# Optimization experiments

Measured on AMD Instinct MI355X. Metric: run time of the kernel, lower is better.

Reference implementation:

```python
import jax, jax.numpy as jnp
import numpy as np

NEG_INF = -9e15  # matches torch masked_fill value


def setup_inputs() -> dict:
    key = jax.random.key(0)
    k1, k2 = jax.random.split(key)
    N, D = 8192, 512
    cxr_feats = jax.random.normal(k1, (N, D), dtype=jnp.float32)
    ehr_feats = jax.random.normal(k2, (N, D), dtype=jnp.float32)
    temperature = jnp.float32(0.07)
    return {"cxr_feats": cxr_feats, "ehr_feats": ehr_feats, "temperature": temperature}


def reference(cxr_feats, ehr_feats, temperature):
    # Fused L2-normalize + GEMM instead of broadcast cosine_similarity.
    eps = 1e-8  # torch cosine_similarity eps default
    cxr_n = cxr_feats / jnp.maximum(jnp.linalg.norm(cxr_feats, axis=-1, keepdims=True), eps)
    ehr_n = ehr_feats / jnp.maximum(jnp.linalg.norm(ehr_feats, axis=-1, keepdims=True), eps)
    cos_sim = jnp.einsum('nd,md->nm', cxr_n, ehr_n) / temperature  # [N, N]
    N = cos_sim.shape[0]
    diag = jnp.diagonal(cos_sim)  # positives
    self_mask = jnp.eye(N, dtype=bool)
    cos_sim_neg = jnp.where(self_mask, NEG_INF, cos_sim)
    nll_1 = diag - jax.scipy.special.logsumexp(cos_sim_neg, axis=1)
    nll_2 = diag - jax.scipy.special.logsumexp(cos_sim_neg, axis=0)
    loss = -(nll_1 + nll_2).mean()
    return loss
```

## Files before the change

kernel.cpp:

```cpp
#include <hip/hip_runtime.h>
#include <hip/hip_bf16.h>

#define N_ROWS 8192
#define D_DIM  512
#define NSTEPS 8

typedef __attribute__((ext_vector_type(4))) int   i32x4;
typedef __attribute__((ext_vector_type(8))) int   i32x8;
typedef __attribute__((ext_vector_type(16))) float f32x16;

typedef const __attribute__((address_space(1))) void* gptr_t;
typedef __attribute__((address_space(3))) void* lptr_t;

static __device__ __forceinline__ void gload16(const void* g, void* l) {
    __builtin_amdgcn_global_load_lds((gptr_t)g, (lptr_t)l, 16, 0, 0);
}
#define VMCNT(n)  asm volatile("s_waitcnt vmcnt(" #n ")" ::: "memory")
#define BARRIER() __builtin_amdgcn_s_barrier()
#define SCHED0()  __builtin_amdgcn_sched_barrier(0)

__global__ void normdiag_kernel(const float* __restrict__ cxr, const float* __restrict__ ehr,
                                unsigned char* __restrict__ Ab, unsigned char* __restrict__ Bb,
                                const float* __restrict__ temp, float* __restrict__ dg) {
    const int row = blockIdx.x * 4 + (threadIdx.x >> 6);
    const int lane = threadIdx.x & 63;
    const float4* a4 = (const float4*)(cxr + (size_t)row * D_DIM + lane * 8);
    const float4* b4 = (const float4*)(ehr + (size_t)row * D_DIM + lane * 8);
    float4 a0 = a4[0], a1 = a4[1];
    float4 b0 = b4[0], b1 = b4[1];
    float sa = a0.x*a0.x + a0.y*a0.y + a0.z*a0.z + a0.w*a0.w
             + a1.x*a1.x + a1.y*a1.y + a1.z*a1.z + a1.w*a1.w;
    float sb = b0.x*b0.x + b0.y*b0.y + b0.z*b0.z + b0.w*b0.w
             + b1.x*b1.x + b1.y*b1.y + b1.z*b1.z + b1.w*b1.w;
    float dt = a0.x*b0.x + a0.y*b0.y + a0.z*b0.z + a0.w*b0.w
             + a1.x*b1.x + a1.y*b1.y + a1.z*b1.z + a1.w*b1.w;
#pragma unroll
    for (int s = 1; s < 64; s <<= 1) {
        sa += __shfl_xor(sa, s);
        sb += __shfl_xor(sb, s);
        dt += __shfl_xor(dt, s);
    }
    const float ia = 1.0f / sqrtf(fmaxf(sa, 1e-16f));
    const float ib = 1.0f / sqrtf(fmaxf(sb, 1e-16f));
    if (lane == 0) dg[row] = dt * ia * ib / temp[0];
    float va[8] = {a0.x, a0.y, a0.z, a0.w, a1.x, a1.y, a1.z, a1.w};
    float vb[8] = {b0.x, b0.y, b0.z, b0.w, b1.x, b1.y, b1.z, b1.w};
    int aw0 = __builtin_amdgcn_cvt_pk_fp8_f32(va[0]*ia, va[1]*ia, 0, false);
    aw0     = __builtin_amdgcn_cvt_pk_fp8_f32(va[2]*ia, va[3]*ia, aw0, true);
    int aw1 = __builtin_amdgcn_cvt_pk_fp8_f32(va[4]*ia, va[5]*ia, 0, false);
    aw1     = __builtin_amdgcn_cvt_pk_fp8_f32(va[6]*ia, va[7]*ia, aw1, true);
    int bw0 = __builtin_amdgcn_cvt_pk_fp8_f32(vb[0]*ib, vb[1]*ib, 0, false);
    bw0     = __builtin_amdgcn_cvt_pk_fp8_f32(vb[2]*ib, vb[3]*ib, bw0, true);
    int bw1 = __builtin_amdgcn_cvt_pk_fp8_f32(vb[4]*ib, vb[5]*ib, 0, false);
    bw1     = __builtin_amdgcn_cvt_pk_fp8_f32(vb[6]*ib, vb[7]*ib, bw1, true);
    *(int2*)(Ab + (size_t)row * D_DIM + lane * 8) = make_int2(aw0, aw1);
    *(int2*)(Bb + (size_t)row * D_DIM + lane * 8) = make_int2(bw0, bw1);
}

static __device__ __forceinline__ i32x8 ld2(const unsigned char* p0, const unsigned char* p1) {
    i32x4 lo = *(const i32x4*)p0;
    i32x4 hi = *(const i32x4*)(p1);
    return (i32x8){lo[0], lo[1], lo[2], lo[3], hi[0], hi[1], hi[2], hi[3]};
}

__global__ __launch_bounds__(512, 2) void gemm_lse_kernel(
        const unsigned char* __restrict__ A, const unsigned char* __restrict__ B,
        const float* __restrict__ temp,
        float* __restrict__ row_sum, float* __restrict__ col_sum) {
    __shared__ unsigned char As[3][8192];
    __shared__ unsigned char Bs[3][8192];

    const int tid = threadIdx.x;
    const int lane = tid & 63;
    const int wid = tid >> 6;
    const int bm = blockIdx.x & 63;
    const int bn = blockIdx.x >> 6;
    const int wm = wid >> 2, wn = wid & 3;

    const int swz = ((lane & 3) ^ ((lane >> 3) & 3)) * 16;
    const unsigned char* gA = A + (size_t)(bm * 128 + wid * 16 + (lane >> 2)) * D_DIM + swz;
    const unsigned char* gB = B + (size_t)(bn * 128 + wid * 16 + (lane >> 2)) * D_DIM + swz;

#define STG(d, st) do { \
    gload16(gA + (st) * 64, &As[d][(wid * 16) * 64]); \
    gload16(gB + (st) * 64, &Bs[d][(wid * 16) * 64]); } while (0)

    const int c31 = lane & 31, h2 = lane >> 5;
    const int so0 = (((2 * h2) ^ ((c31 >> 1) & 3)) & 3) * 16;

    f32x16 acc[2] = {};
    f32x16 accT[2] = {};
    const int sc = 0x7F7F7F7F;

    STG(0, 0);
    STG(1, 1);
    VMCNT(2);
    BARRIER(); SCHED0();

#pragma unroll
    for (int s = 0; s < NSTEPS; ++s) {
        const int d = s % 3;
        if (s + 2 < NSTEPS) STG((s + 2) % 3, s + 2);

        i32x8 Af0, Af1, Bf;
        {
            const unsigned char* rp = &As[d][(wm * 64 + c31) * 64];
            Af0 = ld2(rp + so0, rp + (so0 ^ 16));
            rp += 32 * 64;
            Af1 = ld2(rp + so0, rp + (so0 ^ 16));
            const unsigned char* bp = &Bs[d][(wn * 32 + c31) * 64];
            Bf = ld2(bp + so0, bp + (so0 ^ 16));
        }
        acc[0]  = __builtin_amdgcn_mfma_scale_f32_32x32x64_f8f6f4(Af0, Bf, acc[0],  0, 0, 0, sc, 0, sc);
        acc[1]  = __builtin_amdgcn_mfma_scale_f32_32x32x64_f8f6f4(Af1, Bf, acc[1],  0, 0, 0, sc, 0, sc);
        accT[0] = __builtin_amdgcn_mfma_scale_f32_32x32x64_f8f6f4(Bf, Af0, accT[0], 0, 0, 0, sc, 0, sc);
        accT[1] = __builtin_amdgcn_mfma_scale_f32_32x32x64_f8f6f4(Bf, Af1, accT[1], 0, 0, 0, sc, 0, sc);

        if (s <= NSTEPS - 3)       { VMCNT(2); BARRIER(); SCHED0(); }
        else if (s == NSTEPS - 2)  { VMCNT(0); BARRIER(); SCHED0(); }
    }

    const float c1 = 1.4426950408889634f / temp[0];
    const float c0 = -c1;
    const bool dBlk = (bm == bn);

    float csum = 0.f;
#pragma unroll
    for (int mi = 0; mi < 2; ++mi) {
        f32x16 a = acc[mi];
#pragma unroll
        for (int r = 0; r < 16; ++r) {
            float e = exp2f(fmaf(a[r], c1, c0));
            if (dBlk) {
                int grow = wm * 64 + mi * 32 + (r & 3) + 8 * (r >> 2) + 4 * h2;
                int gcol = wn * 32 + c31;
                if (grow == gcol) e = 0.f;
            }
            csum += e;
        }
    }
    csum += __shfl_xor(csum, 32);
    if (h2 == 0) atomicAdd(&col_sum[bn * 128 + wn * 32 + c31], csum);

#pragma unroll
    for (int mi = 0; mi < 2; ++mi) {
        f32x16 a = accT[mi];
        float rsum = 0.f;
#pragma unroll
        for (int r = 0; r < 16; ++r) {
            float e = exp2f(fmaf(a[r], c1, c0));
            if (dBlk) {
                int grow = wn * 32 + (r & 3) + 8 * (r >> 2) + 4 * h2;
                int gcol = wm * 64 + mi * 32 + c31;
                if (grow == gcol) e = 0.f;
            }
            rsum += e;
        }
        rsum += __shfl_xor(rsum, 32);
        if (h2 == 0) atomicAdd(&row_sum[bm * 128 + wm * 64 + mi * 32 + c31], rsum);
    }
}

__global__ void finalize_kernel(const float* __restrict__ rs, const float* __restrict__ cs,
                                const float* __restrict__ dg, const float* __restrict__ temp,
                                float* __restrict__ out) {
    const float M = 1.0f / temp[0];
    const int i = blockIdx.x * 512 + threadIdx.x;
    float acc = 2.f * M + __logf(rs[i]) + __logf(cs[i]) - 2.f * dg[i];
#pragma unroll
    for (int s = 1; s < 64; s <<= 1) acc += __shfl_xor(acc, s);
    __shared__ float wsum[8];
    if ((threadIdx.x & 63) == 0) wsum[threadIdx.x >> 6] = acc;
    __syncthreads();
    if (threadIdx.x == 0) {
        float t = 0.f;
#pragma unroll
        for (int w = 0; w < 8; ++w) t += wsum[w];
        atomicAdd(out, t / (float)N_ROWS);
    }
}

extern "C" void kernel_launch(void* const* d_in, const int* in_sizes, int n_in,
                              void* d_out, int out_size, void* d_ws, size_t ws_size,
                              hipStream_t stream) {
    const float* cxr = (const float*)d_in[0];
    const float* ehr = (const float*)d_in[1];
    const float* temp = (const float*)d_in[2];
    float* out = (float*)d_out;

    char* ws = (char*)d_ws;
    unsigned char* Ab = (unsigned char*)ws;
    unsigned char* Bb = (unsigned char*)(ws + 4u * 1024 * 1024);
    float* rs = (float*)(ws + 8u * 1024 * 1024);
    float* cs = rs + N_ROWS;
    float* dg = cs + N_ROWS;

    hipMemsetAsync(rs, 0, 2 * N_ROWS * sizeof(float), stream);
    hipMemsetAsync(out, 0, sizeof(float), stream);
    normdiag_kernel<<<dim3(N_ROWS / 4), 256, 0, stream>>>(cxr, ehr, Ab, Bb, temp, dg);
    gemm_lse_kernel<<<dim3(64 * 64), 512, 0, stream>>>(Ab, Bb, temp, rs, cs);
    finalize_kernel<<<dim3(16), 512, 0, stream>>>(rs, cs, dg, temp, out);
}
```

Baseline: 99.56 us.

## Use 4 waves per block with 64x64 per-wave tiles in fused GEMM-LSE

Halves the block to 256 threads (4 waves, 2x2 grid) and gives each wave a 64x64 output sub-tile with a 2x2 set of MFMA accumulators plus their transposes, instead of 64x32 with 8 waves. Each wave now loads two A and two B fragments per step and issues 8 MFMAs, which improves register-level reuse of LDS fragments and cuts duplicate B loads. Staging issues four global-to-LDS loads per thread to cover the same 128-row tiles, with wait counts adjusted. The cost is double the accumulator registers per wave (128 AGPR/VGPR for accumulators) and fewer waves resident to hide latency.

```diff
diff --git a/kernel.cpp b/kernel.cpp
--- a/kernel.cpp
+++ b/kernel.cpp
@@ -63,7 +63,7 @@
     return (i32x8){lo[0], lo[1], lo[2], lo[3], hi[0], hi[1], hi[2], hi[3]};
 }
 
-__global__ __launch_bounds__(512, 2) void gemm_lse_kernel(
+__global__ __launch_bounds__(256, 2) void gemm_lse_kernel(
         const unsigned char* __restrict__ A, const unsigned char* __restrict__ B,
         const float* __restrict__ temp,
         float* __restrict__ row_sum, float* __restrict__ col_sum) {
@@ -75,26 +75,28 @@
     const int wid = tid >> 6;
     const int bm = blockIdx.x & 63;
     const int bn = blockIdx.x >> 6;
-    const int wm = wid >> 2, wn = wid & 3;
+    const int wm = wid >> 1, wn = wid & 1;
 
     const int swz = ((lane & 3) ^ ((lane >> 3) & 3)) * 16;
-    const unsigned char* gA = A + (size_t)(bm * 128 + wid * 16 + (lane >> 2)) * D_DIM + swz;
-    const unsigned char* gB = B + (size_t)(bn * 128 + wid * 16 + (lane >> 2)) * D_DIM + swz;
+    const unsigned char* gA = A + (size_t)(bm * 128 + wid * 32 + (lane >> 2)) * D_DIM + swz;
+    const unsigned char* gB = B + (size_t)(bn * 128 + wid * 32 + (lane >> 2)) * D_DIM + swz;
 
 #define STG(d, st) do { \
-    gload16(gA + (st) * 64, &As[d][(wid * 16) * 64]); \
-    gload16(gB + (st) * 64, &Bs[d][(wid * 16) * 64]); } while (0)
+    gload16(gA + (st) * 64,                &As[d][(wid * 32) * 64]); \
+    gload16(gA + 16 * D_DIM + (st) * 64,   &As[d][(wid * 32 + 16) * 64]); \
+    gload16(gB + (st) * 64,                &Bs[d][(wid * 32) * 64]); \
+    gload16(gB + 16 * D_DIM + (st) * 64,   &Bs[d][(wid * 32 + 16) * 64]); } while (0)
 
     const int c31 = lane & 31, h2 = lane >> 5;
     const int so0 = (((2 * h2) ^ ((c31 >> 1) & 3)) & 3) * 16;
 
-    f32x16 acc[2] = {};
-    f32x16 accT[2] = {};
+    f32x16 acc[2][2] = {};
+    f32x16 accT[2][2] = {};
     const int sc = 0x7F7F7F7F;
 
     STG(0, 0);
     STG(1, 1);
-    VMCNT(2);
+    VMCNT(4);
     BARRIER(); SCHED0();
 
 #pragma unroll
@@ -102,21 +104,27 @@
         const int d = s % 3;
         if (s + 2 < NSTEPS) STG((s + 2) % 3, s + 2);
 
-        i32x8 Af0, Af1, Bf;
+        i32x8 Af0, Af1, Bf0, Bf1;
         {
             const unsigned char* rp = &As[d][(wm * 64 + c31) * 64];
             Af0 = ld2(rp + so0, rp + (so0 ^ 16));
             rp += 32 * 64;
             Af1 = ld2(rp + so0, rp + (so0 ^ 16));
-            const unsigned char* bp = &Bs[d][(wn * 32 + c31) * 64];
-            Bf = ld2(bp + so0, bp + (so0 ^ 16));
+            const unsigned char* bp = &Bs[d][(wn * 64 + c31) * 64];
+            Bf0 = ld2(bp + so0, bp + (so0 ^ 16));
+            bp += 32 * 64;
+            Bf1 = ld2(bp + so0, bp + (so0 ^ 16));
         }
-        acc[0]  = __builtin_amdgcn_mfma_scale_f32_32x32x64_f8f6f4(Af0, Bf, acc[0],  0, 0, 0, sc, 0, sc);
-        acc[1]  = __builtin_amdgcn_mfma_scale_f32_32x32x64_f8f6f4(Af1, Bf, acc[1],  0, 0, 0, sc, 0, sc);
-        accT[0] = __builtin_amdgcn_mfma_scale_f32_32x32x64_f8f6f4(Bf, Af0, accT[0], 0, 0, 0, sc, 0, sc);
-        accT[1] = __builtin_amdgcn_mfma_scale_f32_32x32x64_f8f6f4(Bf, Af1, accT[1], 0, 0, 0, sc, 0, sc);
-
-        if (s <= NSTEPS - 3)       { VMCNT(2); BARRIER(); SCHED0(); }
+        acc[0][0]  = __builtin_amdgcn_mfma_scale_f32_32x32x64_f8f6f4(Af0, Bf0, acc[0][0],  0, 0, 0, sc, 0, sc);
+        accT[0][0] = __builtin_amdgcn_mfma_scale_f32_32x32x64_f8f6f4(Bf0, Af0, accT[0][0], 0, 0, 0, sc, 0, sc);
+        acc[0][1]  = __builtin_amdgcn_mfma_scale_f32_32x32x64_f8f6f4(Af0, Bf1, acc[0][1],  0, 0, 0, sc, 0, sc);
+        accT[1][0] = __builtin_amdgcn_mfma_scale_f32_32x32x64_f8f6f4(Bf1, Af0, accT[1][0], 0, 0, 0, sc, 0, sc);
+        acc[1][0]  = __builtin_amdgcn_mfma_scale_f32_32x32x64_f8f6f4(Af1, Bf0, acc[1][0],  0, 0, 0, sc, 0, sc);
+        accT[0][1] = __builtin_amdgcn_mfma_scale_f32_32x32x64_f8f6f4(Bf0, Af1, accT[0][1], 0, 0, 0, sc, 0, sc);
+        acc[1][1]  = __builtin_amdgcn_mfma_scale_f32_32x32x64_f8f6f4(Af1, Bf1, acc[1][1],  0, 0, 0, sc, 0, sc);
+        accT[1][1] = __builtin_amdgcn_mfma_scale_f32_32x32x64_f8f6f4(Bf1, Af1, accT[1][1], 0, 0, 0, sc, 0, sc);
+
+        if (s <= NSTEPS - 3)       { VMCNT(4); BARRIER(); SCHED0(); }
         else if (s == NSTEPS - 2)  { VMCNT(0); BARRIER(); SCHED0(); }
     }
 
@@ -124,37 +132,43 @@
     const float c0 = -c1;
     const bool dBlk = (bm == bn);
 
-    float csum = 0.f;
+#pragma unroll
+    for (int ni = 0; ni < 2; ++ni) {
+        float csum = 0.f;
+#pragma unroll
+        for (int mi = 0; mi < 2; ++mi) {
+            f32x16 a = acc[mi][ni];
+#pragma unroll
+            for (int r = 0; r < 16; ++r) {
+                float e = exp2f(fmaf(a[r], c1, c0));
+                if (dBlk) {
+                    int grow = wm * 64 + mi * 32 + (r & 3) + 8 * (r >> 2) + 4 * h2;
+                    int gcol = wn * 64 + ni * 32 + c31;
+                    if (grow == gcol) e = 0.f;
+                }
+                csum += e;
+            }
+        }
+        csum += __shfl_xor(csum, 32);
+        if (h2 == 0) atomicAdd(&col_sum[bn * 128 + wn * 64 + ni * 32 + c31], csum);
+    }
+
 #pragma unroll
     for (int mi = 0; mi < 2; ++mi) {
-        f32x16 a = acc[mi];
-#pragma unroll
-        for (int r = 0; r < 16; ++r) {
-            float e = exp2f(fmaf(a[r], c1, c0));
-            if (dBlk) {
-                int grow = wm * 64 + mi * 32 + (r & 3) + 8 * (r >> 2) + 4 * h2;
-                int gcol = wn * 32 + c31;
-                if (grow == gcol) e = 0.f;
+        float rsum = 0.f;
+#pragma unroll
+        for (int ni = 0; ni < 2; ++ni) {
+            f32x16 a = accT[ni][mi];
+#pragma unroll
+            for (int r = 0; r < 16; ++r) {
+                float e = exp2f(fmaf(a[r], c1, c0));
+                if (dBlk) {
+                    int grow = wn * 64 + ni * 32 + (r & 3) + 8 * (r >> 2) + 4 * h2;
+                    int gcol = wm * 64 + mi * 32 + c31;
+                    if (grow == gcol) e = 0.f;
+                }
+                rsum += e;
             }
-            csum += e;
-        }
-    }
-    csum += __shfl_xor(csum, 32);
-    if (h2 == 0) atomicAdd(&col_sum[bn * 128 + wn * 32 + c31], csum);
-
-#pragma unroll
-    for (int mi = 0; mi < 2; ++mi) {
-        f32x16 a = accT[mi];
-        float rsum = 0.f;
-#pragma unroll
-        for (int r = 0; r < 16; ++r) {
-            float e = exp2f(fmaf(a[r], c1, c0));
-            if (dBlk) {
-                int grow = wn * 32 + (r & 3) + 8 * (r >> 2) + 4 * h2;
-                int gcol = wm * 64 + mi * 32 + c31;
-                if (grow == gcol) e = 0.f;
-            }
-            rsum += e;
         }
         rsum += __shfl_xor(rsum, 32);
         if (h2 == 0) atomicAdd(&row_sum[bm * 128 + wm * 64 + mi * 32 + c31], rsum);
@@ -198,6 +212,6 @@
     hipMemsetAsync(rs, 0, 2 * N_ROWS * sizeof(float), stream);
     hipMemsetAsync(out, 0, sizeof(float), stream);
     normdiag_kernel<<<dim3(N_ROWS / 4), 256, 0, stream>>>(cxr, ehr, Ab, Bb, temp, dg);
-    gemm_lse_kernel<<<dim3(64 * 64), 512, 0, stream>>>(Ab, Bb, temp, rs, cs);
+    gemm_lse_kernel<<<dim3(64 * 64), 256, 0, stream>>>(Ab, Bb, temp, rs, cs);
     finalize_kernel<<<dim3(16), 512, 0, stream>>>(rs, cs, dg, temp, out);
 }
```

New measurement: 101.8 us. +2.2%, slower.
